# Optimization experiments

Hardware: AMD Instinct MI355X
Metric: run time of the kernel (lower is better)

Reference implementation:

```python
import jax, jax.numpy as jnp
import numpy as np

EMBED_DIM = 1024
N_HEADS = 16
HEAD_DIM = EMBED_DIM // N_HEADS
B, T = 4, 2048
LN_EPS = 1e-5


def layernorm(x, gamma, beta):
    mu = jnp.mean(x, axis=-1, keepdims=True)
    var = jnp.var(x, axis=-1, keepdims=True)
    return (x - mu) * jax.lax.rsqrt(var + LN_EPS) * gamma + beta


def setup_inputs() -> dict:
    key = jax.random.key(0)
    ks = jax.random.split(key, 12)
    s = 0.02
    C, H, HD, F = EMBED_DIM, N_HEADS, HEAD_DIM, 4 * EMBED_DIM
    return {
        "x": jax.random.normal(ks[0], (B, T, C), dtype=jnp.float32),
        "Wq": jax.random.normal(ks[1], (H, C, HD), dtype=jnp.float32) * s,
        "Wk": jax.random.normal(ks[2], (H, C, HD), dtype=jnp.float32) * s,
        "Wv": jax.random.normal(ks[3], (H, C, HD), dtype=jnp.float32) * s,
        "Wo": jax.random.normal(ks[4], (C, C), dtype=jnp.float32) * s,
        "bo": jnp.zeros((C,), dtype=jnp.float32),
        "g1": jnp.ones((C,), dtype=jnp.float32),
        "beta1": jnp.zeros((C,), dtype=jnp.float32),
        "g2": jnp.ones((C,), dtype=jnp.float32),
        "beta2": jnp.zeros((C,), dtype=jnp.float32),
        "W1": jax.random.normal(ks[5], (C, F), dtype=jnp.float32) * s,
        "bff1": jnp.zeros((F,), dtype=jnp.float32),
        "W2": jax.random.normal(ks[6], (F, C), dtype=jnp.float32) * s,
        "bff2": jnp.zeros((C,), dtype=jnp.float32),
    }


def reference(x, Wq, Wk, Wv, Wo, bo, g1, beta1, g2, beta2, W1, bff1, W2, bff2):
    Bx, Tx, C = x.shape
    norm_x = layernorm(x, g1, beta1)
    # per-head projections (no bias), stacked: [B, H, T, HD]
    q = jnp.einsum("btc,hcd->bhtd", norm_x, Wq)
    k = jnp.einsum("btc,hcd->bhtd", norm_x, Wk)
    v = jnp.einsum("btc,hcd->bhtd", norm_x, Wv)
    scale = 1.0 / np.sqrt(HEAD_DIM).astype(np.float32)
    scores = jnp.einsum("bhtd,bhsd->bhts", q, k) * scale  # [B,H,T,T]
    causal = jnp.tril(jnp.ones((Tx, Tx), dtype=bool))
    scores = jnp.where(causal, scores, -jnp.inf)
    probs = jax.nn.softmax(scores, axis=-1)
    attn = jnp.einsum("bhts,bhsd->bhtd", probs, v)  # [B,H,T,HD]
    # concat heads -> [B, T, H*HD] then output linear
    attn = jnp.transpose(attn, (0, 2, 1, 3)).reshape(Bx, Tx, C)
    attn_out = attn @ Wo + bo
    res = x + attn_out
    norm_res = layernorm(res, g2, beta2)
    h = jax.nn.gelu(norm_res @ W1 + bff1, approximate=False)
    ffn = h @ W2 + bff2
    return res + ffn
```

## Files before the change

### kernel.cpp

```cpp
#include <hip/hip_runtime.h>
#include <math.h>

constexpr int Bsz = 4, T = 2048, C = 1024, H = 16, HD = 64, F = 4096;
constexpr int M = Bsz * T;
constexpr int NT = T / 64;

typedef _Float16 f16x8 __attribute__((ext_vector_type(8)));
typedef float f32x4 __attribute__((ext_vector_type(4)));
typedef unsigned int u32;

__device__ __forceinline__ void async_copy16(void* lds, const void* g) {
  __builtin_amdgcn_global_load_lds((const __attribute__((address_space(1))) u32*)g,
                                   (__attribute__((address_space(3))) u32*)lds, 16, 0, 0);
}

union H4 { _Float16 h[4]; uint2 u; };

__global__ __launch_bounds__(256) void ln_kernel(const float* __restrict__ x,
                                                 const float* __restrict__ g,
                                                 const float* __restrict__ b,
                                                 _Float16* __restrict__ outh) {
  const int row = blockIdx.x;
  const int tid = threadIdx.x;
  const float4 v = ((const float4*)(x + (size_t)row * C))[tid];
  float s = v.x + v.y + v.z + v.w;
  float ss = v.x * v.x + v.y * v.y + v.z * v.z + v.w * v.w;
#pragma unroll
  for (int off = 32; off > 0; off >>= 1) {
    s += __shfl_xor(s, off, 64);
    ss += __shfl_xor(ss, off, 64);
  }
  __shared__ float red[2][4];
  const int wv = tid >> 6;
  if ((tid & 63) == 0) { red[0][wv] = s; red[1][wv] = ss; }
  __syncthreads();
  s = red[0][0] + red[0][1] + red[0][2] + red[0][3];
  ss = red[1][0] + red[1][1] + red[1][2] + red[1][3];
  const float mu = s * (1.0f / C);
  const float var = ss * (1.0f / C) - mu * mu;
  const float rstd = rsqrtf(var + 1e-5f);
  const float4 gv = ((const float4*)g)[tid];
  const float4 bv = ((const float4*)b)[tid];
  H4 pk;
  pk.h[0] = (_Float16)((v.x - mu) * rstd * gv.x + bv.x);
  pk.h[1] = (_Float16)((v.y - mu) * rstd * gv.y + bv.y);
  pk.h[2] = (_Float16)((v.z - mu) * rstd * gv.z + bv.z);
  pk.h[3] = (_Float16)((v.w - mu) * rstd * gv.w + bv.w);
  ((uint2*)(outh + (size_t)row * C))[tid] = pk.u;
}

__global__ __launch_bounds__(256) void tconv(const float* __restrict__ W,
                                             _Float16* __restrict__ WT,
                                             int K, int N) {
  __shared__ float tile[64][65];
  const int tid = threadIdx.x;
  const int n0 = blockIdx.x * 64, k0 = blockIdx.y * 64;
#pragma unroll
  for (int i = 0; i < 4; ++i) {
    const int idx = i * 1024 + tid * 4;
    const int r = idx >> 6, c = idx & 63;
    const float4 v = *(const float4*)&W[(size_t)(k0 + r) * N + n0 + c];
    tile[r][c] = v.x; tile[r][c + 1] = v.y; tile[r][c + 2] = v.z; tile[r][c + 3] = v.w;
  }
  __syncthreads();
#pragma unroll
  for (int i = 0; i < 4; ++i) {
    const int idx = i * 1024 + tid * 4;
    const int r = idx >> 6, c = idx & 63;
    H4 pk;
#pragma unroll
    for (int j = 0; j < 4; ++j) pk.h[j] = (_Float16)tile[c + j][r];
    *(uint2*)&WT[(size_t)(n0 + r) * K + k0 + c] = pk.u;
  }
}

__global__ __launch_bounds__(256) void tconv_qkv(const float* __restrict__ Wq,
                                                 const float* __restrict__ Wk,
                                                 const float* __restrict__ Wv,
                                                 _Float16* __restrict__ WcatT) {
  __shared__ float tile[64][65];
  const int tid = threadIdx.x;
  const int c0 = blockIdx.x * 64;
  const int h = blockIdx.y, wsel = blockIdx.z;
  const float* W = (wsel == 0 ? Wq : (wsel == 1 ? Wk : Wv)) + (size_t)h * C * HD;
  const int base_row = wsel * 1024 + h * 64;
#pragma unroll
  for (int i = 0; i < 4; ++i) {
    const int idx = i * 1024 + tid * 4;
    const int r = idx >> 6, c = idx & 63;
    const float4 v = *(const float4*)&W[(size_t)(c0 + r) * HD + c];
    tile[r][c] = v.x; tile[r][c + 1] = v.y; tile[r][c + 2] = v.z; tile[r][c + 3] = v.w;
  }
  __syncthreads();
#pragma unroll
  for (int i = 0; i < 4; ++i) {
    const int idx = i * 1024 + tid * 4;
    const int r = idx >> 6, c = idx & 63;
    H4 pk;
#pragma unroll
    for (int j = 0; j < 4; ++j) pk.h[j] = (_Float16)tile[c + j][r];
    *(uint2*)&WcatT[(size_t)(base_row + r) * C + c0 + c] = pk.u;
  }
}

template <int MODE>
__global__ __launch_bounds__(256) void mgemm(const _Float16* __restrict__ Ah,
                                             const _Float16* __restrict__ Bh,
                                             const float* __restrict__ bias,
                                             const float* __restrict__ resid,
                                             float* __restrict__ Of,
                                             _Float16* __restrict__ Oh,
                                             _Float16* __restrict__ Oh2,
                                             _Float16* __restrict__ Oh3,
                                             int Ndim, int Kdim) {
  __shared__ _Float16 Alds[128 * 64];
  __shared__ _Float16 Blds[128 * 64];
  const int tid = threadIdx.x;
  const int wv = tid >> 6, ln = tid & 63;
  const int wm = wv >> 1, wn = wv & 1;
  int bx = blockIdx.x, by = blockIdx.y;
  {
    const int gx = gridDim.x;
    const int nwg = gx * gridDim.y;
    if ((nwg & 7) == 0) {
      int wg = by * gx + bx;
      wg = (wg & 7) * (nwg >> 3) + (wg >> 3);
      bx = wg % gx;
      by = wg / gx;
    }
  }
  const int m0 = by * 128, n0 = bx * 128;
  const int lr = ln & 15, lk = ln >> 4;

  const _Float16* Abase = Ah + (size_t)m0 * Kdim;
  const _Float16* Bbase = Bh + (size_t)n0 * Kdim;

  f32x4 acc[4][4] = {};

  for (int k0 = 0; k0 < Kdim; k0 += 64) {
    __syncthreads();
#pragma unroll
    for (int i = 0; i < 4; ++i) {
      const int seg = wv * 4 + i;
      const int row = seg * 8 + (ln >> 3);
      async_copy16(Alds + seg * 512, Abase + (size_t)row * Kdim + k0 + (ln & 7) * 8);
      async_copy16(Blds + seg * 512, Bbase + (size_t)row * Kdim + k0 + (ln & 7) * 8);
    }
    __syncthreads();
#pragma unroll
    for (int kk = 0; kk < 2; ++kk) {
      f16x8 af[4], bf[4];
#pragma unroll
      for (int fm = 0; fm < 4; ++fm)
        af[fm] = *(const f16x8*)&Alds[(wm * 64 + fm * 16 + lr) * 64 + kk * 32 + lk * 8];
#pragma unroll
      for (int fn = 0; fn < 4; ++fn)
        bf[fn] = *(const f16x8*)&Blds[(wn * 64 + fn * 16 + lr) * 64 + kk * 32 + lk * 8];
      __builtin_amdgcn_s_setprio(1);
#pragma unroll
      for (int fm = 0; fm < 4; ++fm)
#pragma unroll
        for (int fn = 0; fn < 4; ++fn)
          acc[fm][fn] = __builtin_amdgcn_mfma_f32_16x16x32_f16(af[fm], bf[fn], acc[fm][fn], 0, 0, 0);
      __builtin_amdgcn_s_setprio(0);
    }
  }

#pragma unroll
  for (int fm = 0; fm < 4; ++fm) {
#pragma unroll
    for (int fn = 0; fn < 4; ++fn) {
      const int row0 = m0 + wm * 64 + fm * 16 + lk * 4;
      const int col = n0 + wn * 64 + fn * 16 + lr;
      const f32x4 v = acc[fm][fn];
      if (MODE == 0) {
        const int wsel = col >> 10, h = (col >> 6) & 15, d = col & 63;
#pragma unroll
        for (int r = 0; r < 4; ++r) {
          const int m = row0 + r;
          const int bb = m >> 11, t = m & (T - 1);
          if (wsel == 0)
            Oh[(((size_t)bb * H + h) * T + t) * HD + d] = (_Float16)(v[r] * 0.18033688011112042f);
          else if (wsel == 1)
            Oh2[(((size_t)bb * H + h) * T + t) * HD + d] = (_Float16)v[r];
          else
            Oh3[(((size_t)bb * H + h) * HD + d) * T + t] = (_Float16)v[r];
        }
      } else if (MODE == 1 || MODE == 3) {
        const float bc = bias[col];
#pragma unroll
        for (int r = 0; r < 4; ++r)
          Of[(size_t)(row0 + r) * Ndim + col] =
              v[r] + bc + resid[(size_t)(row0 + r) * Ndim + col];
      } else {
        const float bc = bias[col];
#pragma unroll
        for (int r = 0; r < 4; ++r) {
          float t = v[r] + bc;
          t = 0.5f * t * (1.0f + erff(t * 0.70710678118654752f));
          Oh[(size_t)(row0 + r) * Ndim + col] = (_Float16)t;
        }
      }
    }
  }
}

__device__ __forceinline__ void qkt_tile(const f16x8 (&qf)[2],
                                         const _Float16* __restrict__ Kbuf,
                                         f32x4 (&s)[4], int lr, int lk) {
  __builtin_amdgcn_s_setprio(1);
#pragma unroll
  for (int ct = 0; ct < 4; ++ct) {
    s[ct] = f32x4{0.f, 0.f, 0.f, 0.f};
#pragma unroll
    for (int kk = 0; kk < 2; ++kk) {
      const int row = ct * 16 + lr;
      const int ch = (kk * 4 + lk) ^ (row & 7);
      const f16x8 kf = *(const f16x8*)&Kbuf[row * 64 + ch * 8];
      s[ct] = __builtin_amdgcn_mfma_f32_16x16x32_f16(qf[kk], kf, s[ct], 0, 0, 0);
    }
  }
  __builtin_amdgcn_s_setprio(0);
}

__device__ __forceinline__ void online_sm(f32x4 (&s)[4], float (&m_i)[4], float (&l_i)[4],
                                          f32x4 (&acc)[4], _Float16 (&ph)[4][4]) {
  float alpha[4];
#pragma unroll
  for (int r = 0; r < 4; ++r) {
    float mx = fmaxf(fmaxf(s[0][r], s[1][r]), fmaxf(s[2][r], s[3][r]));
#pragma unroll
    for (int off = 1; off < 16; off <<= 1) mx = fmaxf(mx, __shfl_xor(mx, off, 16));
    const float mn = fmaxf(m_i[r], mx);
    alpha[r] = exp2f(m_i[r] - mn);
    m_i[r] = mn;
  }
  float rs[4] = {0.f, 0.f, 0.f, 0.f};
#pragma unroll
  for (int ct = 0; ct < 4; ++ct)
#pragma unroll
    for (int r = 0; r < 4; ++r) {
      const float p = exp2f(s[ct][r] - m_i[r]);
      rs[r] += p;
      ph[ct][r] = (_Float16)p;
    }
#pragma unroll
  for (int r = 0; r < 4; ++r) {
#pragma unroll
    for (int off = 1; off < 16; off <<= 1) rs[r] += __shfl_xor(rs[r], off, 16);
    l_i[r] = l_i[r] * alpha[r] + rs[r];
#pragma unroll
    for (int dt = 0; dt < 4; ++dt) acc[dt][r] *= alpha[r];
  }
}

__device__ __forceinline__ void pv_tile(const _Float16 (&ph)[4][4], _Float16* Pb,
                                        const _Float16* __restrict__ Vbuf,
                                        f32x4 (&acc)[4], int w, int lr, int lk) {
#pragma unroll
  for (int ct = 0; ct < 4; ++ct)
#pragma unroll
    for (int r = 0; r < 4; ++r) {
      const int q = w * 16 + lk * 4 + r;
      const int kv = ct * 16 + lr;
      Pb[q * 64 + (kv ^ ((q & 7) * 8))] = ph[ct][r];
    }
  const int qrow = w * 16 + lr;
  __builtin_amdgcn_s_setprio(1);
#pragma unroll
  for (int kk = 0; kk < 2; ++kk) {
    const int pch = (kk * 4 + lk) ^ (qrow & 7);
    const f16x8 pa = *(const f16x8*)&Pb[qrow * 64 + pch * 8];
#pragma unroll
    for (int dt = 0; dt < 4; ++dt) {
      const int drow = dt * 16 + lr;
      const int vch = (kk * 4 + lk) ^ (drow & 7);
      const f16x8 vf = *(const f16x8*)&Vbuf[drow * 64 + vch * 8];
      acc[dt] = __builtin_amdgcn_mfma_f32_16x16x32_f16(pa, vf, acc[dt], 0, 0, 0);
    }
  }
  __builtin_amdgcn_s_setprio(0);
}

__global__ __launch_bounds__(256) void attn_mfma(const _Float16* __restrict__ Qh,
                                                 const _Float16* __restrict__ Kh,
                                                 const _Float16* __restrict__ Vth,
                                                 _Float16* __restrict__ O) {
  __shared__ _Float16 Kb[2][64 * 64];
  __shared__ _Float16 Vb[2][64 * 64];
  __shared__ _Float16 Pb[64 * 64];
  const int tid = threadIdx.x;
  const int w = tid >> 6, l = tid & 63;
  const int lr = l & 15, lk = l >> 4;
  const int qlo = blockIdx.x, qhi = (NT - 1) - blockIdx.x;
  const int bh = blockIdx.y;
  const _Float16* Qg = Qh + (size_t)bh * T * HD;
  const _Float16* Kg = Kh + (size_t)bh * T * HD;
  const _Float16* Vg = Vth + (size_t)bh * HD * T;

  f16x8 qfl[2], qfh[2];
#pragma unroll
  for (int kk = 0; kk < 2; ++kk) {
    qfl[kk] = *(const f16x8*)&Qg[(size_t)(qlo * 64 + w * 16 + lr) * HD + kk * 32 + lk * 8];
    qfh[kk] = *(const f16x8*)&Qg[(size_t)(qhi * 64 + w * 16 + lr) * HD + kk * 32 + lk * 8];
  }

  f32x4 accl[4] = {}, acch[4] = {};
  float ml[4], ll[4], mh[4], lh[4];
#pragma unroll
  for (int r = 0; r < 4; ++r) {
    ml[r] = -INFINITY; ll[r] = 0.f;
    mh[r] = -INFINITY; lh[r] = 0.f;
  }

  const int srow = l >> 3;
  const int schunk = (l & 7) ^ srow;

  int buf = 0;
#pragma unroll
  for (int i = 0; i < 2; ++i) {
    const int seg = w * 2 + i;
    const int rr = seg * 8 + srow;
    async_copy16(&Kb[0][seg * 512], Kg + (size_t)rr * HD + schunk * 8);
    async_copy16(&Vb[0][seg * 512], Vg + (size_t)rr * T + schunk * 8);
  }

  for (int kt = 0; kt <= qhi; ++kt) {
    __syncthreads();
    if (kt < qhi) {
#pragma unroll
      for (int i = 0; i < 2; ++i) {
        const int seg = w * 2 + i;
        const int rr = seg * 8 + srow;
        async_copy16(&Kb[buf ^ 1][seg * 512],
                     Kg + (size_t)((kt + 1) * 64 + rr) * HD + schunk * 8);
        async_copy16(&Vb[buf ^ 1][seg * 512],
                     Vg + (size_t)rr * T + (kt + 1) * 64 + schunk * 8);
      }
    }
    f32x4 s[4];
    _Float16 ph[4][4];
    qkt_tile(qfh, &Kb[buf][0], s, lr, lk);
    if (kt == qhi) {
#pragma unroll
      for (int ct = 0; ct < 4; ++ct)
#pragma unroll
        for (int r = 0; r < 4; ++r)
          if (ct * 16 + lr > w * 16 + lk * 4 + r) s[ct][r] = -INFINITY;
    }
    online_sm(s, mh, lh, acch, ph);
    pv_tile(ph, &Pb[0], &Vb[buf][0], acch, w, lr, lk);
    if (kt <= qlo) {
      qkt_tile(qfl, &Kb[buf][0], s, lr, lk);
      if (kt == qlo) {
#pragma unroll
        for (int ct = 0; ct < 4; ++ct)
#pragma unroll
          for (int r = 0; r < 4; ++r)
            if (ct * 16 + lr > w * 16 + lk * 4 + r) s[ct][r] = -INFINITY;
      }
      online_sm(s, ml, ll, accl, ph);
      pv_tile(ph, &Pb[0], &Vb[buf][0], accl, w, lr, lk);
    }
    buf ^= 1;
  }
  const int bb = bh >> 4, h = bh & 15;
#pragma unroll
  for (int r = 0; r < 4; ++r) {
    const float invh = 1.0f / lh[r];
    const int th = qhi * 64 + w * 16 + lk * 4 + r;
#pragma unroll
    for (int dt = 0; dt < 4; ++dt)
      O[((size_t)bb * T + th) * C + h * 64 + dt * 16 + lr] = (_Float16)(acch[dt][r] * invh);
    const float invl = 1.0f / ll[r];
    const int tl = qlo * 64 + w * 16 + lk * 4 + r;
#pragma unroll
    for (int dt = 0; dt < 4; ++dt)
      O[((size_t)bb * T + tl) * C + h * 64 + dt * 16 + lr] = (_Float16)(accl[dt][r] * invl);
  }
}

extern "C" void kernel_launch(void* const* d_in, const int* in_sizes, int n_in,
                              void* d_out, int out_size, void* d_ws, size_t ws_size,
                              hipStream_t stream) {
  (void)in_sizes; (void)n_in; (void)out_size; (void)ws_size;
  const float* x   = (const float*)d_in[0];
  const float* Wq  = (const float*)d_in[1];
  const float* Wk  = (const float*)d_in[2];
  const float* Wv  = (const float*)d_in[3];
  const float* Wo  = (const float*)d_in[4];
  const float* bo  = (const float*)d_in[5];
  const float* g1  = (const float*)d_in[6];
  const float* be1 = (const float*)d_in[7];
  const float* g2  = (const float*)d_in[8];
  const float* be2 = (const float*)d_in[9];
  const float* W1  = (const float*)d_in[10];
  const float* b1  = (const float*)d_in[11];
  const float* W2  = (const float*)d_in[12];
  const float* b2  = (const float*)d_in[13];
  float* out = (float*)d_out;

  char* base = (char*)d_ws;
  _Float16* norm_h = (_Float16*)base;
  _Float16* WcatT  = (_Float16*)(base + (16ull << 20));
  _Float16* WoT    = (_Float16*)(base + (22ull << 20));
  _Float16* W1T    = (_Float16*)(base + (24ull << 20));
  _Float16* W2T    = (_Float16*)(base + (32ull << 20));
  _Float16* Qhb    = (_Float16*)(base + (40ull << 20));
  _Float16* Khb    = (_Float16*)(base + (56ull << 20));
  _Float16* Vthb   = (_Float16*)(base + (72ull << 20));
  _Float16* attnCh = (_Float16*)(base + (88ull << 20));
  float* res       = (float*)(base + (104ull << 20));
  _Float16* hbuf   = (_Float16*)(base + (40ull << 20));

  tconv_qkv<<<dim3(16, 16, 3), 256, 0, stream>>>(Wq, Wk, Wv, WcatT);
  tconv<<<dim3(16, 16), 256, 0, stream>>>(Wo, WoT, C, C);
  tconv<<<dim3(64, 16), 256, 0, stream>>>(W1, W1T, C, F);
  tconv<<<dim3(16, 64), 256, 0, stream>>>(W2, W2T, F, C);

  ln_kernel<<<M, 256, 0, stream>>>(x, g1, be1, norm_h);
  mgemm<0><<<dim3(3072 / 128, M / 128), 256, 0, stream>>>(
      norm_h, WcatT, nullptr, nullptr, nullptr, Qhb, Khb, Vthb, 3072, C);
  attn_mfma<<<dim3(NT / 2, Bsz * H), 256, 0, stream>>>(Qhb, Khb, Vthb, attnCh);
  mgemm<1><<<dim3(C / 128, M / 128), 256, 0, stream>>>(
      attnCh, WoT, bo, x, res, nullptr, nullptr, nullptr, C, C);
  ln_kernel<<<M, 256, 0, stream>>>(res, g2, be2, norm_h);
  mgemm<2><<<dim3(F / 128, M / 128), 256, 0, stream>>>(
      norm_h, W1T, b1, nullptr, nullptr, hbuf, nullptr, nullptr, F, C);
  mgemm<3><<<dim3(C / 128, M / 128), 256, 0, stream>>>(
      hbuf, W2T, b2, res, out, nullptr, nullptr, nullptr, C, F);
}
```

Baseline: 644.1 us.

## Transpose QK^T fragment layout and skip small online-softmax rescales

Swaps the MFMA operands in the QK^T tile so each lane holds scores for a single query row. The row max and row sum then need only two cross-lane shuffles instead of four per row, and the running max and sum shrink to one scalar per lane. It also adds lazy rescaling: when no row's max grows by more than 8 (in log2 units), the previous max is kept and the accumulator rescale is skipped. The cost is extra shuffles to send alpha and the final sums to the output layout, and a wave-wide vote on every tile.

```diff
diff --git a/kernel.cpp b/kernel.cpp
--- a/kernel.cpp
+++ b/kernel.cpp
@@ -217,60 +217,64 @@
       const int row = ct * 16 + lr;
       const int ch = (kk * 4 + lk) ^ (row & 7);
       const f16x8 kf = *(const f16x8*)&Kbuf[row * 64 + ch * 8];
-      s[ct] = __builtin_amdgcn_mfma_f32_16x16x32_f16(qf[kk], kf, s[ct], 0, 0, 0);
+      s[ct] = __builtin_amdgcn_mfma_f32_16x16x32_f16(kf, qf[kk], s[ct], 0, 0, 0);
     }
   }
   __builtin_amdgcn_s_setprio(0);
 }
 
-__device__ __forceinline__ void online_sm(f32x4 (&s)[4], float (&m_i)[4], float (&l_i)[4],
-                                          f32x4 (&acc)[4], _Float16 (&ph)[4][4]) {
-  float alpha[4];
-#pragma unroll
-  for (int r = 0; r < 4; ++r) {
-    float mx = fmaxf(fmaxf(s[0][r], s[1][r]), fmaxf(s[2][r], s[3][r]));
-#pragma unroll
-    for (int off = 1; off < 16; off <<= 1) mx = fmaxf(mx, __shfl_xor(mx, off, 16));
-    const float mn = fmaxf(m_i[r], mx);
-    alpha[r] = exp2f(m_i[r] - mn);
-    m_i[r] = mn;
-  }
-  float rs[4] = {0.f, 0.f, 0.f, 0.f};
+__device__ __forceinline__ void online_sm(const f32x4 (&s)[4], float& m_i, float& l_i,
+                                          f32x4 (&acc)[4], _Float16 (&ph)[4][4], int l) {
+  float mx = fmaxf(fmaxf(s[0][0], s[0][1]), fmaxf(s[0][2], s[0][3]));
+#pragma unroll
+  for (int ct = 1; ct < 4; ++ct)
+    mx = fmaxf(mx, fmaxf(fmaxf(s[ct][0], s[ct][1]), fmaxf(s[ct][2], s[ct][3])));
+  mx = fmaxf(mx, __shfl_xor(mx, 16, 64));
+  mx = fmaxf(mx, __shfl_xor(mx, 32, 64));
+  float mn = fmaxf(m_i, mx);
+  if (__all(mx - m_i <= 8.0f)) {
+    mn = m_i;
+  } else {
+    const float alpha = exp2f(m_i - mn);
+    m_i = mn;
+    l_i *= alpha;
+#pragma unroll
+    for (int r = 0; r < 4; ++r) {
+      const float a_r = __shfl(alpha, (l & 48) | (((l >> 4) & 3) * 4 + r), 64);
+#pragma unroll
+      for (int dt = 0; dt < 4; ++dt) acc[dt][r] *= a_r;
+    }
+  }
+  float rs = 0.f;
 #pragma unroll
   for (int ct = 0; ct < 4; ++ct)
 #pragma unroll
     for (int r = 0; r < 4; ++r) {
-      const float p = exp2f(s[ct][r] - m_i[r]);
-      rs[r] += p;
+      const float p = exp2f(s[ct][r] - mn);
+      rs += p;
       ph[ct][r] = (_Float16)p;
     }
-#pragma unroll
-  for (int r = 0; r < 4; ++r) {
-#pragma unroll
-    for (int off = 1; off < 16; off <<= 1) rs[r] += __shfl_xor(rs[r], off, 16);
-    l_i[r] = l_i[r] * alpha[r] + rs[r];
-#pragma unroll
-    for (int dt = 0; dt < 4; ++dt) acc[dt][r] *= alpha[r];
-  }
+  rs += __shfl_xor(rs, 16, 64);
+  rs += __shfl_xor(rs, 32, 64);
+  l_i += rs;
 }
 
 __device__ __forceinline__ void pv_tile(const _Float16 (&ph)[4][4], _Float16* Pb,
                                         const _Float16* __restrict__ Vbuf,
                                         f32x4 (&acc)[4], int w, int lr, int lk) {
+  const int qw = w * 16 + lr;
 #pragma unroll
   for (int ct = 0; ct < 4; ++ct)
 #pragma unroll
     for (int r = 0; r < 4; ++r) {
-      const int q = w * 16 + lk * 4 + r;
-      const int kv = ct * 16 + lr;
-      Pb[q * 64 + (kv ^ ((q & 7) * 8))] = ph[ct][r];
-    }
-  const int qrow = w * 16 + lr;
+      const int kv = ct * 16 + lk * 4 + r;
+      Pb[qw * 64 + (kv ^ ((qw & 7) * 8))] = ph[ct][r];
+    }
   __builtin_amdgcn_s_setprio(1);
 #pragma unroll
   for (int kk = 0; kk < 2; ++kk) {
-    const int pch = (kk * 4 + lk) ^ (qrow & 7);
-    const f16x8 pa = *(const f16x8*)&Pb[qrow * 64 + pch * 8];
+    const int pch = (kk * 4 + lk) ^ (qw & 7);
+    const f16x8 pa = *(const f16x8*)&Pb[qw * 64 + pch * 8];
 #pragma unroll
     for (int dt = 0; dt < 4; ++dt) {
       const int drow = dt * 16 + lr;
@@ -306,12 +310,7 @@
   }
 
   f32x4 accl[4] = {}, acch[4] = {};
-  float ml[4], ll[4], mh[4], lh[4];
-#pragma unroll
-  for (int r = 0; r < 4; ++r) {
-    ml[r] = -INFINITY; ll[r] = 0.f;
-    mh[r] = -INFINITY; lh[r] = 0.f;
-  }
+  float ml = -INFINITY, ll = 0.f, mh = -INFINITY, lh = 0.f;
 
   const int srow = l >> 3;
   const int schunk = (l & 7) ^ srow;
@@ -346,9 +345,9 @@
       for (int ct = 0; ct < 4; ++ct)
 #pragma unroll
         for (int r = 0; r < 4; ++r)
-          if (ct * 16 + lr > w * 16 + lk * 4 + r) s[ct][r] = -INFINITY;
-    }
-    online_sm(s, mh, lh, acch, ph);
+          if (ct * 16 + lk * 4 + r > w * 16 + lr) s[ct][r] = -INFINITY;
+    }
+    online_sm(s, mh, lh, acch, ph, l);
     pv_tile(ph, &Pb[0], &Vb[buf][0], acch, w, lr, lk);
     if (kt <= qlo) {
       qkt_tile(qfl, &Kb[buf][0], s, lr, lk);
@@ -357,9 +356,9 @@
         for (int ct = 0; ct < 4; ++ct)
 #pragma unroll
           for (int r = 0; r < 4; ++r)
-            if (ct * 16 + lr > w * 16 + lk * 4 + r) s[ct][r] = -INFINITY;
+            if (ct * 16 + lk * 4 + r > w * 16 + lr) s[ct][r] = -INFINITY;
       }
-      online_sm(s, ml, ll, accl, ph);
+      online_sm(s, ml, ll, accl, ph, l);
       pv_tile(ph, &Pb[0], &Vb[buf][0], accl, w, lr, lk);
     }
     buf ^= 1;
@@ -367,12 +366,14 @@
   const int bb = bh >> 4, h = bh & 15;
 #pragma unroll
   for (int r = 0; r < 4; ++r) {
-    const float invh = 1.0f / lh[r];
+    const float lh_r = __shfl(lh, (l & 48) | (lk * 4 + r), 64);
+    const float invh = 1.0f / lh_r;
     const int th = qhi * 64 + w * 16 + lk * 4 + r;
 #pragma unroll
     for (int dt = 0; dt < 4; ++dt)
       O[((size_t)bb * T + th) * C + h * 64 + dt * 16 + lr] = (_Float16)(acch[dt][r] * invh);
-    const float invl = 1.0f / ll[r];
+    const float ll_r = __shfl(ll, (l & 48) | (lk * 4 + r), 64);
+    const float invl = 1.0f / ll_r;
     const int tl = qlo * 64 + w * 16 + lk * 4 + r;
 #pragma unroll
     for (int dt = 0; dt < 4; ++dt)
```

After: 616.0 us. 1.05x faster.
